# Kernel tuning notes

Measured on AMD Instinct MI355X. Metric: run time of the kernel, lower is better.

## Reference

```python
import jax, jax.numpy as jnp
import numpy as np

B, S, D, H, FFN = 2, 2048, 1024, 8, 4096
DK = D // H            # head key/query dim = 128
VD = 2 * D             # double_v_dim -> v_dim = 2048
DV = VD // H           # per-head value dim = 256
SCALE_BASE = 512.0
EPS = 1e-5


def _dup_interleave(m):
    # (S, d/2) -> (S, d), each column repeated twice adjacently
    return jnp.repeat(m, 2, axis=-1)


def _rotate_every_two(x):
    x1 = x[..., 0::2]
    x2 = x[..., 1::2]
    return jnp.stack((-x2, x1), axis=-1).reshape(x.shape)


def _xpos(x, downscale):
    # x: (B,H,S,d) -- XPOS rotary with length-dependent scale
    d = x.shape[-1]
    pos = jnp.arange(x.shape[-2], dtype=jnp.float32)
    sv = (jnp.arange(0, d, 2, dtype=jnp.float32) + 0.4 * d) / (1.4 * d)  # (d/2,)
    scale = sv[None, :] ** (pos / SCALE_BASE)[:, None]                    # (S, d/2)
    half = d // 2
    inv_freq = 1.0 / (10000.0 ** (jnp.arange(half, dtype=jnp.float32) / half))
    sinusoid = pos[:, None] * inv_freq[None, :]                           # (S, d/2)
    if downscale:
        scale = 1.0 / scale
    sin = _dup_interleave(jnp.sin(sinusoid) * scale)                      # (S, d)
    cos = _dup_interleave(jnp.cos(sinusoid) * scale)
    return x * cos + _rotate_every_two(x) * sin


def _gammas(heads):
    return 1.0 - jnp.exp(jnp.linspace(np.log(1 / 32), np.log(1 / 512), heads)).astype(jnp.float32)


def _layernorm(x, w, b):
    mu = jnp.mean(x, axis=-1, keepdims=True)
    var = jnp.var(x, axis=-1, keepdims=True)
    return (x - mu) * jax.lax.rsqrt(var + EPS) * w + b


def setup_inputs() -> dict:
    key = jax.random.key(0)
    ks = jax.random.split(key, 16)
    sD = 1.0 / np.sqrt(D)
    sF = 1.0 / np.sqrt(FFN)
    return {
        "X": jax.random.normal(ks[0], (B, S, D), jnp.float32),
        "Wq": jax.random.normal(ks[1], (H, D, DK), jnp.float32) * sD,
        "Wk": jax.random.normal(ks[2], (H, D, DK), jnp.float32) * sD,
        "Wv": jax.random.normal(ks[3], (H, D, DV), jnp.float32) * sD,
        "W_G": jax.random.normal(ks[4], (D, VD), jnp.float32) * sD,
        "W_O": jax.random.normal(ks[5], (VD, D), jnp.float32) / np.sqrt(VD),
        "gn_w": jnp.ones((VD,), jnp.float32),
        "gn_b": jnp.zeros((VD,), jnp.float32),
        "ln1_w": jnp.ones((D,), jnp.float32),
        "ln1_b": jnp.zeros((D,), jnp.float32),
        "ln2_w": jnp.ones((D,), jnp.float32),
        "ln2_b": jnp.zeros((D,), jnp.float32),
        "ffn_w1": jax.random.normal(ks[6], (D, FFN), jnp.float32) * sD,
        "ffn_b1": jnp.zeros((FFN,), jnp.float32),
        "ffn_w2": jax.random.normal(ks[7], (FFN, D), jnp.float32) * sF,
        "ffn_b2": jnp.zeros((D,), jnp.float32),
    }


def _retention(Xn, Wq, Wk, Wv, W_G, W_O, gn_w, gn_b):
    # Xn: (B,S,D) pre-normalized input
    Q = jnp.einsum("bsd,hdk->bhsk", Xn, Wq)
    K = jnp.einsum("bsd,hdk->bhsk", Xn, Wk)
    V = jnp.einsum("bsd,hdv->bhsv", Xn, Wv)
    Q = _xpos(Q, downscale=False)
    K = _xpos(K, downscale=True)
    # decay matrix D[h,n,m] = gamma_h^(n-m) for n>=m else 0
    n = jnp.arange(S)[:, None]
    m = jnp.arange(S)[None, :]
    mask = (n >= m)
    exponent = jnp.where(mask, (n - m).astype(jnp.float32), 0.0)
    g = _gammas(H)
    Dmat = jnp.where(mask[None], g[:, None, None] ** exponent[None], 0.0)  # (H,S,S)
    ret = jnp.einsum("bhsk,bhtk->bhst", Q, K) * Dmat[None]
    Y = jnp.einsum("bhst,bhtv->bhsv", ret, V)                              # (B,H,S,DV)
    Y = jnp.transpose(Y, (0, 2, 1, 3))                                     # (B,S,H,DV)
    # GroupNorm(heads, v_dim) applied per token: normalize within each head chunk
    mu = jnp.mean(Y, axis=-1, keepdims=True)
    var = jnp.var(Y, axis=-1, keepdims=True)
    Y = (Y - mu) * jax.lax.rsqrt(var + EPS)
    Y = Y.reshape(B, S, VD) * gn_w + gn_b
    G = Xn @ W_G
    gated = (G * jax.nn.sigmoid(G)) * Y                                     # swish gate
    return gated @ W_O


def reference(X, Wq, Wk, Wv, W_G, W_O, gn_w, gn_b, ln1_w, ln1_b, ln2_w, ln2_b,
              ffn_w1, ffn_b1, ffn_w2, ffn_b2):
    X = _retention(_layernorm(X, ln1_w, ln1_b), Wq, Wk, Wv, W_G, W_O, gn_w, gn_b) + X
    h = _layernorm(X, ln2_w, ln2_b)
    h = jax.nn.gelu(h @ ffn_w1 + ffn_b1, approximate=False) @ ffn_w2 + ffn_b2
    return h + X
```

## Files before the change

kernel.cpp:

```cpp
#include <hip/hip_runtime.h>
#include <hip/hip_bf16.h>

typedef unsigned short u16;
typedef unsigned int   u32;
typedef short short8 __attribute__((ext_vector_type(8)));
typedef float f32x4  __attribute__((ext_vector_type(4)));

__device__ __forceinline__ float b2f(u16 u) { return __uint_as_float(((u32)u) << 16); }
__device__ __forceinline__ u16 f2b(float f) {
    u32 u = __float_as_uint(f);
    u += 0x7FFF + ((u >> 16) & 1);
    return (u16)(u >> 16);
}

typedef const unsigned int __attribute__((address_space(1)))* gas1;
typedef unsigned int __attribute__((address_space(3)))* las3;
__device__ __forceinline__ void async_ld16(const void* g, const void* l) {
    __builtin_amdgcn_global_load_lds((gas1)(unsigned long long)g,
                                     (las3)(unsigned int)(unsigned long long)l,
                                     16, 0, 0);
}

__device__ __forceinline__ void wtrans_body(const float* __restrict__ W, u16* __restrict__ Wt,
                                            int K, int N, int bx, int by, int bz) {
    __shared__ u16 tile[32][36];
    const int k0 = bx * 32, n0 = by * 32;
    const float* Wz = W + (long)bz * K * N;
    u16* Wtz = Wt + (long)bz * K * N;
    const int t = threadIdx.x;
    const int r = t >> 3, c = (t & 7) * 4;
    float4 v = *(const float4*)(Wz + (long)(k0 + r) * N + n0 + c);
    tile[r][c+0] = f2b(v.x); tile[r][c+1] = f2b(v.y);
    tile[r][c+2] = f2b(v.z); tile[r][c+3] = f2b(v.w);
    __syncthreads();
    uint2 pk;
    pk.x = (u32)tile[c+0][r] | ((u32)tile[c+1][r] << 16);
    pk.y = (u32)tile[c+2][r] | ((u32)tile[c+3][r] << 16);
    *(uint2*)(Wtz + (long)(n0 + r) * K + k0 + c) = pk;
}

__device__ __forceinline__ void xtab_body(float4* __restrict__ tab, int blk) {
    int idx = blk * 256 + threadIdx.x;
    int j = idx & 63, s = idx >> 6;
    float sv = (2.f * j + 51.2f) / 179.2f;
    float scale = exp2f(log2f(sv) * ((float)s * (1.f / 512.f)));
    float inv_freq = exp2f((float)j * (-13.287712379549449f / 64.f));
    float ang = (float)s * inv_freq;
    float sn = sinf(ang), cs = cosf(ang);
    tab[idx] = make_float4(cs * scale, sn * scale, cs / scale, sn / scale);
}

__device__ __forceinline__ void ln_body(const float* __restrict__ X,
                                        const float* __restrict__ w,
                                        const float* __restrict__ bb,
                                        u16* __restrict__ out, long row) {
    const int t = threadIdx.x;
    float4 p = ((const float4*)(X + row * 1024))[t];
    float x[4] = { p.x, p.y, p.z, p.w };
    float s = x[0]+x[1]+x[2]+x[3];
    float q = x[0]*x[0]+x[1]*x[1]+x[2]*x[2]+x[3]*x[3];
#pragma unroll
    for (int o = 32; o > 0; o >>= 1) { s += __shfl_down(s, o, 64); q += __shfl_down(q, o, 64); }
    __shared__ float aS[4], aQ[4];
    if ((t & 63) == 0) { aS[t >> 6] = s; aQ[t >> 6] = q; }
    __syncthreads();
    s = aS[0]+aS[1]+aS[2]+aS[3];
    q = aQ[0]+aQ[1]+aQ[2]+aQ[3];
    float mean = s * (1.f/1024.f);
    float var  = q * (1.f/1024.f) - mean*mean;
    float rstd = rsqrtf(var + 1e-5f);
    float4 wv = ((const float4*)w)[t];
    float4 bv = ((const float4*)bb)[t];
    uint2 r;
    r.x = (u32)f2b((x[0]-mean)*rstd*wv.x + bv.x) | ((u32)f2b((x[1]-mean)*rstd*wv.y + bv.y) << 16);
    r.y = (u32)f2b((x[2]-mean)*rstd*wv.z + bv.z) | ((u32)f2b((x[3]-mean)*rstd*wv.w + bv.w) << 16);
    ((uint2*)(out + row * 1024))[t] = r;
}

__global__ __launch_bounds__(256) void prep_k(
    const float* __restrict__ Wq, const float* __restrict__ Wk,
    const float* __restrict__ Wv, const float* __restrict__ WG,
    const float* __restrict__ WO, const float* __restrict__ fw1,
    const float* __restrict__ fw2, const float* __restrict__ X,
    const float* __restrict__ ln1w, const float* __restrict__ ln1b,
    u16* __restrict__ WT, u16* __restrict__ WOT,
    u16* __restrict__ fw1T, u16* __restrict__ fw2T,
    float4* __restrict__ xtab, u16* __restrict__ Xn) {
    const int id = blockIdx.x;
    if (id < 16384) {
        const float* W; u16* Wt; int K, N, bx, by, bz = 0;
        if (id < 1024)       { W=Wq;  Wt=WT;           K=1024; N=128;  int l=id;       bx=l&31;  by=(l>>5)&3; bz=l>>7; }
        else if (id < 2048)  { W=Wk;  Wt=WT+1048576;   K=1024; N=128;  int l=id-1024;  bx=l&31;  by=(l>>5)&3; bz=l>>7; }
        else if (id < 4096)  { W=Wv;  Wt=WT+2097152;   K=1024; N=256;  int l=id-2048;  bx=l&31;  by=(l>>5)&7; bz=l>>8; }
        else if (id < 6144)  { W=WG;  Wt=WT+4194304;   K=1024; N=2048; int l=id-4096;  bx=l&31;  by=l>>5; }
        else if (id < 8192)  { W=WO;  Wt=WOT;          K=2048; N=1024; int l=id-6144;  bx=l&63;  by=l>>6; }
        else if (id < 12288) { W=fw1; Wt=fw1T;         K=1024; N=4096; int l=id-8192;  bx=l&31;  by=l>>5; }
        else                 { W=fw2; Wt=fw2T;         K=4096; N=1024; int l=id-12288; bx=l&127; by=l>>7; }
        wtrans_body(W, Wt, K, N, bx, by, bz);
    } else if (id < 16896) {
        xtab_body(xtab, id - 16384);
    } else {
        ln_body(X, ln1w, ln1b, Xn, id - 16896);
    }
}

__global__ __launch_bounds__(256) void ln2_combine(const float* __restrict__ P,
                                                   const float* __restrict__ X,
                                                   const float* __restrict__ w,
                                                   const float* __restrict__ bb,
                                                   float* __restrict__ X2,
                                                   u16* __restrict__ hb) {
    const long row = blockIdx.x;
    const int t = threadIdx.x;
    const float* p = P + row * 3072;
    float4 a = ((const float4*)p)[t];
    float4 c = ((const float4*)(p + 1024))[t];
    float4 xr = ((const float4*)(X + row * 1024))[t];
    float x[4] = { a.x+c.x+xr.x, a.y+c.y+xr.y, a.z+c.z+xr.z, a.w+c.w+xr.w };
    ((float4*)(X2 + row * 1024))[t] = make_float4(x[0], x[1], x[2], x[3]);
    float s = x[0]+x[1]+x[2]+x[3];
    float q = x[0]*x[0]+x[1]*x[1]+x[2]*x[2]+x[3]*x[3];
#pragma unroll
    for (int o = 32; o > 0; o >>= 1) { s += __shfl_down(s, o, 64); q += __shfl_down(q, o, 64); }
    __shared__ float aS[4], aQ[4];
    if ((t & 63) == 0) { aS[t >> 6] = s; aQ[t >> 6] = q; }
    __syncthreads();
    s = aS[0]+aS[1]+aS[2]+aS[3];
    q = aQ[0]+aQ[1]+aQ[2]+aQ[3];
    float mean = s * (1.f/1024.f);
    float var  = q * (1.f/1024.f) - mean*mean;
    float rstd = rsqrtf(var + 1e-5f);
    float4 wv = ((const float4*)w)[t];
    float4 bv = ((const float4*)bb)[t];
    uint2 r;
    r.x = (u32)f2b((x[0]-mean)*rstd*wv.x + bv.x) | ((u32)f2b((x[1]-mean)*rstd*wv.y + bv.y) << 16);
    r.y = (u32)f2b((x[2]-mean)*rstd*wv.z + bv.z) | ((u32)f2b((x[3]-mean)*rstd*wv.w + bv.w) << 16);
    ((uint2*)(hb + row * 1024))[t] = r;
}

__global__ __launch_bounds__(256) void ffn2_combine(const float* __restrict__ P,
                                                    const float* __restrict__ b2,
                                                    const float* __restrict__ X2,
                                                    float* __restrict__ out) {
    const long row = blockIdx.x;
    const int t = threadIdx.x;
    float4 p0 = ((const float4*)(P + row * 1024))[t];
    float4 p1 = ((const float4*)(P + 16777216 + row * 1024))[t];
    float4 x2 = ((const float4*)(X2 + row * 1024))[t];
    float4 bv = ((const float4*)b2)[t];
    ((float4*)(out + row * 1024))[t] = make_float4(
        p0.x + p1.x + x2.x + bv.x, p0.y + p1.y + x2.y + bv.y,
        p0.z + p1.z + x2.z + bv.z, p0.w + p1.w + x2.w + bv.w);
}

__global__ __launch_bounds__(256) void vtrans(const u16* __restrict__ Vseg, u16* __restrict__ Vt) {
    __shared__ u16 tile[32][36];
    const int s0 = blockIdx.x * 32, v0 = blockIdx.y * 32, z = blockIdx.z;
    const int b = z >> 3, h = z & 7;
    const u16* Vz = Vseg + (long)b * 2048 * 6144 + h * 256;
    u16* Vtz = Vt + (long)z * 256 * 2048;
    const int t = threadIdx.x;
    const int r = t >> 3, c = (t & 7) * 4;
    uint2 ld = *(const uint2*)(Vz + (long)(s0 + r) * 6144 + v0 + c);
    tile[r][c+0] = (u16)(ld.x & 0xFFFF); tile[r][c+1] = (u16)(ld.x >> 16);
    tile[r][c+2] = (u16)(ld.y & 0xFFFF); tile[r][c+3] = (u16)(ld.y >> 16);
    __syncthreads();
    uint2 pk;
    pk.x = (u32)tile[c+0][r] | ((u32)tile[c+1][r] << 16);
    pk.y = (u32)tile[c+2][r] | ((u32)tile[c+3][r] << 16);
    *(uint2*)(Vtz + (long)(v0 + r) * 2048 + s0 + c) = pk;
}

enum { EPI_GELU_BIAS = 2, EPI_QKVG = 4 };

template<int EPI, int PANELS>
__global__ __launch_bounds__(256) void mgemm(
    const u16* __restrict__ A, const u16* __restrict__ Bt, u16* __restrict__ Cv,
    int K, int aStride, long cStride,
    const float* __restrict__ bias) {
    __shared__ __align__(16) u16 As[PANELS * 4096];
    __shared__ __align__(16) u16 Bs[PANELS * 4096];
    const int pid = blockIdx.x;
    const int mb = pid & 31;
    const int nb = pid >> 5;
    const int t = threadIdx.x;
    const int row0 = mb * 128, col0 = nb * 128;
    const int wave = t >> 6, lane = t & 63;
    const int wm = wave >> 1, wn = wave & 1;
    const int quad = lane >> 4, l16 = lane & 15;
    const u16* Ag = A + (long)(row0 + (t >> 2)) * aStride + ((t & 3) * 8);
    const u16* Bg = Bt + (long)(col0 + (t >> 2)) * K + ((t & 3) * 8);
    const long aj = (long)64 * aStride;
    const long bj = (long)64 * K;
    const u32 lo = __builtin_amdgcn_readfirstlane((u32)(wave * 1024));

    f32x4 acc[4][4];
#pragma unroll
    for (int i = 0; i < 4; i++)
#pragma unroll
        for (int j = 0; j < 4; j++) acc[i][j] = (f32x4){0.f, 0.f, 0.f, 0.f};

    for (int k0 = 0; k0 < K; k0 += PANELS * 32) {
#pragma unroll
        for (int h = 0; h < PANELS; h++) {
            const u16* Agh = Ag + k0 + h * 32;
            const u16* Bgh = Bg + k0 + h * 32;
            async_ld16(Agh,      (const char*)As + h*8192 + lo);
            async_ld16(Agh + aj, (const char*)As + h*8192 + 4096 + lo);
            async_ld16(Bgh,      (const char*)Bs + h*8192 + lo);
            async_ld16(Bgh + bj, (const char*)Bs + h*8192 + 4096 + lo);
        }
        __syncthreads();
#pragma unroll
        for (int h = 0; h < PANELS; h++) {
            short8 af[4], bf[4];
#pragma unroll
            for (int mt = 0; mt < 4; mt++)
                af[mt] = *(const short8*)(As + h*4096 + (wm*64 + mt*16 + l16) * 32 + quad*8);
#pragma unroll
            for (int nt = 0; nt < 4; nt++)
                bf[nt] = *(const short8*)(Bs + h*4096 + (wn*64 + nt*16 + l16) * 32 + quad*8);
#pragma unroll
            for (int mt = 0; mt < 4; mt++)
#pragma unroll
                for (int nt = 0; nt < 4; nt++)
                    acc[mt][nt] = __builtin_amdgcn_mfma_f32_16x16x32_bf16(af[mt], bf[nt], acc[mt][nt], 0, 0, 0);
        }
        __syncthreads();
    }

#pragma unroll
    for (int mt = 0; mt < 4; mt++) {
#pragma unroll
        for (int reg = 0; reg < 4; reg++) {
            int r = row0 + wm*64 + mt*16 + quad*4 + reg;
#pragma unroll
            for (int nt = 0; nt < 4; nt++) {
                int c = col0 + wn*64 + nt*16 + l16;
                float v = acc[mt][nt][reg];
                if constexpr (EPI == EPI_GELU_BIAS) {
                    v += bias[c];
                    v = 0.5f * v * (1.f + erff(v * 0.70710678118654752f));
                } else if constexpr (EPI == EPI_QKVG) {
                    if (c < 2048) {
                        int j = (c & 127) >> 1;
                        float4 tb = ((const float4*)bias)[((r & 2047) << 6) + j];
                        float cs = (c < 1024) ? tb.x : tb.z;
                        float sn = (c < 1024) ? tb.y : tb.w;
                        float partner = __shfl_xor(v, 1, 64);
                        v = v * cs + ((c & 1) ? partner : -partner) * sn;
                    }
                }
                Cv[(long)r * cStride + c] = f2b(v);
            }
        }
    }
}

__global__ __launch_bounds__(256) void mgemm_sk(
    const u16* __restrict__ A, const u16* __restrict__ Bt, float* __restrict__ P,
    int K, int kHalf, int aStride, long pRowStride, long sliceOff) {
    __shared__ __align__(16) u16 As[2 * 4096];
    __shared__ __align__(16) u16 Bs[2 * 4096];
    const int pid = blockIdx.x;
    const int mb = pid & 31;
    const int nb = (pid & 255) >> 5;
    const int slice = pid >> 8;
    const int t = threadIdx.x;
    const int row0 = mb * 128, col0 = nb * 128;
    const int wave = t >> 6, lane = t & 63;
    const int wm = wave >> 1, wn = wave & 1;
    const int quad = lane >> 4, l16 = lane & 15;
    const u16* Ag = A + (long)(row0 + (t >> 2)) * aStride + ((t & 3) * 8);
    const u16* Bg = Bt + (long)(col0 + (t >> 2)) * K + ((t & 3) * 8);
    const long aj = (long)64 * aStride;
    const long bj = (long)64 * K;
    const u32 lo = __builtin_amdgcn_readfirstlane((u32)(wave * 1024));

    f32x4 acc[4][4];
#pragma unroll
    for (int i = 0; i < 4; i++)
#pragma unroll
        for (int j = 0; j < 4; j++) acc[i][j] = (f32x4){0.f, 0.f, 0.f, 0.f};

    const int kBeg = slice * kHalf, kEnd = kBeg + kHalf;
    for (int k0 = kBeg; k0 < kEnd; k0 += 64) {
#pragma unroll
        for (int h = 0; h < 2; h++) {
            const u16* Agh = Ag + k0 + h * 32;
            const u16* Bgh = Bg + k0 + h * 32;
            async_ld16(Agh,      (const char*)As + h*8192 + lo);
            async_ld16(Agh + aj, (const char*)As + h*8192 + 4096 + lo);
            async_ld16(Bgh,      (const char*)Bs + h*8192 + lo);
            async_ld16(Bgh + bj, (const char*)Bs + h*8192 + 4096 + lo);
        }
        __syncthreads();
#pragma unroll
        for (int h = 0; h < 2; h++) {
            short8 af[4], bf[4];
#pragma unroll
            for (int mt = 0; mt < 4; mt++)
                af[mt] = *(const short8*)(As + h*4096 + (wm*64 + mt*16 + l16) * 32 + quad*8);
#pragma unroll
            for (int nt = 0; nt < 4; nt++)
                bf[nt] = *(const short8*)(Bs + h*4096 + (wn*64 + nt*16 + l16) * 32 + quad*8);
#pragma unroll
            for (int mt = 0; mt < 4; mt++)
#pragma unroll
                for (int nt = 0; nt < 4; nt++)
                    acc[mt][nt] = __builtin_amdgcn_mfma_f32_16x16x32_bf16(af[mt], bf[nt], acc[mt][nt], 0, 0, 0);
        }
        __syncthreads();
    }

    float* Pb = P + slice * sliceOff;
#pragma unroll
    for (int mt = 0; mt < 4; mt++) {
#pragma unroll
        for (int reg = 0; reg < 4; reg++) {
            int r = row0 + wm*64 + mt*16 + quad*4 + reg;
#pragma unroll
            for (int nt = 0; nt < 4; nt++) {
                int c = col0 + wn*64 + nt*16 + l16;
                Pb[(long)r * pRowStride + c] = acc[mt][nt][reg];
            }
        }
    }
}

__global__ __launch_bounds__(256) void retention_mfma(
    u16* __restrict__ QKVG, const u16* __restrict__ Vt,
    const float* __restrict__ gnw, const float* __restrict__ gnb) {
    __shared__ __align__(16) u16 Qs[4][64][32];
    __shared__ __align__(16) u16 Ks[2][4][32][32];
    __shared__ __align__(16) u16 Vs[2][256][32];
    __shared__ u16 Ss[64][40];
    const int id = blockIdx.x;
    const int halfg = id >> 8, r5 = id & 255;
    const int bh = r5 >> 4, i16 = r5 & 15;
    const int tile = halfg ? i16 : 31 - i16;
    const int b = bh >> 3, h = bh & 7;
    const int t = threadIdx.x;
    const int wave = t >> 6, lane = t & 63, quad = lane >> 4, l16 = lane & 15;
    const u32 lo = __builtin_amdgcn_readfirstlane((u32)(wave * 1024));
    const u16* Qbase = QKVG + (long)b * 2048 * 6144 + h * 128;
    const u16* Kbase = Qbase + 1024;
    const u16* Vbase = Vt + (long)(b * 8 + h) * 256 * 2048;
    u16* Gseg = QKVG + (long)b * 2048 * 6144 + 4096 + h * 256;

    float g = 1.f - expf(-3.4657359027997265f + (-0.3960841031771116f) * (float)h);
    float log2g = log2f(g);
    const float gi16 = exp2f(log2g * -16.f);
    const float gi32 = gi16 * gi16;
    const float gf[4] = {1.f, g, g*g, g*g*g};
    const int srow0 = tile*64 + wave*16 + quad*4;
    float drun = exp2f(log2g * (float)(srow0 - l16));

    auto issueKV = [&](int jt, int buf) {
#pragma unroll
        for (int i = 0; i < 2; i++) {
            int c = t + i * 256;
            int ks = c >> 7, row = (c >> 2) & 31, cb = c & 3;
            async_ld16(Kbase + (long)(jt*32 + row) * 6144 + ks*32 + cb*8,
                       (const char*)Ks + buf*8192 + i*4096 + lo);
        }
#pragma unroll
        for (int i = 0; i < 4; i++) {
            int c = t + i * 256;
            int row = c >> 2, cb = c & 3;
            async_ld16(Vbase + (long)row * 2048 + jt*32 + cb*8,
                       (const char*)Vs + buf*16384 + i*4096 + lo);
        }
    };

#pragma unroll
    for (int i = 0; i < 4; i++) {
        int c = t + i * 256;
        int ks = c >> 8, row = (c >> 2) & 63, cb = c & 3;
        async_ld16(Qbase + (long)(tile*64 + row) * 6144 + ks*32 + cb*8,
                   (const char*)Qs + i*4096 + lo);
    }
    issueKV(0, 0);

    float gw[16], gbv[16];
#pragma unroll
    for (int nt = 0; nt < 16; nt++) {
        gw[nt]  = gnw[h*256 + nt*16 + l16];
        gbv[nt] = gnb[h*256 + nt*16 + l16];
    }
    f32x4 oacc[16];
#pragma unroll
    for (int nt = 0; nt < 16; nt++) oacc[nt] = (f32x4){0.f, 0.f, 0.f, 0.f};
    __syncthreads();

    const int njt = 2 * tile + 2;
    for (int jt = 0; jt < njt; jt++) {
        const int cur = jt & 1;
        if (jt + 1 < njt) issueKV(jt + 1, cur ^ 1);
        f32x4 s0 = (f32x4){0.f,0.f,0.f,0.f}, s1 = (f32x4){0.f,0.f,0.f,0.f};
#pragma unroll
        for (int ks = 0; ks < 4; ks++) {
            short8 aq = *(const short8*)&Qs[ks][wave*16 + l16][quad*8];
            short8 b0 = *(const short8*)&Ks[cur][ks][l16][quad*8];
            short8 b1 = *(const short8*)&Ks[cur][ks][16 + l16][quad*8];
            s0 = __builtin_amdgcn_mfma_f32_16x16x32_bf16(aq, b0, s0, 0, 0, 0);
            s1 = __builtin_amdgcn_mfma_f32_16x16x32_bf16(aq, b1, s1, 0, 0, 0);
        }
#pragma unroll
        for (int reg = 0; reg < 4; reg++) {
            int srow = srow0 + reg;
            int tc0 = jt*32 + l16, tc1 = tc0 + 16;
            float dbase = drun * gf[reg];
            float d0 = (srow >= tc0) ? dbase : 0.f;
            float d1 = (srow >= tc1) ? dbase * gi16 : 0.f;
            Ss[wave*16 + quad*4 + reg][l16]      = f2b(s0[reg] * d0);
            Ss[wave*16 + quad*4 + reg][16 + l16] = f2b(s1[reg] * d1);
        }
        drun *= gi32;
        short8 as = *(const short8*)&Ss[wave*16 + l16][quad*8];
#pragma unroll
        for (int nt = 0; nt < 16; nt++) {
            short8 bv = *(const short8*)&Vs[cur][nt*16 + l16][quad*8];
            oacc[nt] = __builtin_amdgcn_mfma_f32_16x16x32_bf16(as, bv, oacc[nt], 0, 0, 0);
        }
        __syncthreads();
    }

#pragma unroll
    for (int reg = 0; reg < 4; reg++) {
        float s = 0.f, q = 0.f;
#pragma unroll
        for (int nt = 0; nt < 16; nt++) { float v = oacc[nt][reg]; s += v; q += v*v; }
#pragma unroll
        for (int m = 1; m < 16; m <<= 1) { s += __shfl_xor(s, m, 16); q += __shfl_xor(q, m, 16); }
        float mean = s * (1.f/256.f);
        float var  = q * (1.f/256.f) - mean*mean;
        float rstd = rsqrtf(var + 1e-5f);
        int srow = srow0 + reg;
        u16* grow = Gseg + (long)srow * 6144;
#pragma unroll
        for (int nt = 0; nt < 16; nt++) {
            float gval = b2f(grow[nt*16 + l16]);
            float y = (oacc[nt][reg] - mean) * rstd * gw[nt] + gbv[nt];
            float sg = gval / (1.f + expf(-gval));
            grow[nt*16 + l16] = f2b(sg * y);
        }
    }
}

extern "C" void kernel_launch(void* const* d_in, const int* in_sizes, int n_in,
                              void* d_out, int out_size, void* d_ws, size_t ws_size,
                              hipStream_t stream) {
    (void)in_sizes; (void)n_in; (void)out_size; (void)ws_size;
    const float* X    = (const float*)d_in[0];
    const float* Wq   = (const float*)d_in[1];
    const float* Wk   = (const float*)d_in[2];
    const float* Wv   = (const float*)d_in[3];
    const float* WG   = (const float*)d_in[4];
    const float* WO   = (const float*)d_in[5];
    const float* gnw  = (const float*)d_in[6];
    const float* gnb  = (const float*)d_in[7];
    const float* ln1w = (const float*)d_in[8];
    const float* ln1b = (const float*)d_in[9];
    const float* ln2w = (const float*)d_in[10];
    const float* ln2b = (const float*)d_in[11];
    const float* fw1  = (const float*)d_in[12];
    const float* fb1  = (const float*)d_in[13];
    const float* fw2  = (const float*)d_in[14];
    const float* fb2  = (const float*)d_in[15];

    constexpr int D = 1024, FFN = 4096;
    constexpr int M = 4096;
    constexpr long MB = 1048576;

    char* ws = (char*)d_ws;
    u16* WT   = (u16*)(ws + 0*MB);
    u16* WOT  = (u16*)(ws + 12*MB);
    u16* fw1T = (u16*)(ws + 16*MB);
    u16* fw2T = (u16*)(ws + 24*MB);
    u16*   QKVG = (u16*)(ws + 32*MB);
    u16*   Xn   = (u16*)(ws + 80*MB);
    float4* xtab= (float4*)(ws + 88*MB);
    u16*   Vt   = (u16*)(ws + 80*MB);
    float* X2   = (float*)(ws + 80*MB);
    u16*   hb   = (u16*)(ws + 0*MB);
    u16*   mid  = (u16*)(ws + 32*MB);
    float* PF   = (float*)(ws + 0*MB);

    prep_k<<<20992, 256, 0, stream>>>(Wq, Wk, Wv, WG, WO, fw1, fw2, X, ln1w, ln1b,
                                      WT, WOT, fw1T, fw2T, xtab, Xn);
    mgemm<EPI_QKVG, 1><<<1536, 256, 0, stream>>>(
        Xn, WT, QKVG, D, D, 6144, (const float*)xtab);
    vtrans<<<dim3(64, 8, 16), 256, 0, stream>>>(QKVG + 2048, Vt);
    retention_mfma<<<512, 256, 0, stream>>>(QKVG, Vt, gnw, gnb);
    mgemm_sk<<<512, 256, 0, stream>>>(
        QKVG + 4096, WOT, (float*)QKVG, 2048, 1024, 6144, 3072, 1024);
    ln2_combine<<<M, 256, 0, stream>>>((const float*)QKVG, X, ln2w, ln2b, X2, hb);
    mgemm<EPI_GELU_BIAS, 2><<<1024, 256, 0, stream>>>(
        hb, fw1T, mid, D, D, FFN, fb1);
    mgemm_sk<<<512, 256, 0, stream>>>(
        mid, fw2T, PF, 4096, 2048, 4096, 1024, 16777216);
    ffn2_combine<<<M, 256, 0, stream>>>(PF, fb2, X2, (float*)d_out);
}
```

Before: 472.3 us.

## Fuse V transpose into QKVG GEMM epilogue and use faster GELU/sigmoid

The QKVG GEMM epilogue now writes V tiles directly in transposed layout to a separate Vt buffer, which removes the standalone vtrans kernel and its round trip through memory. The exact erf GELU is replaced with a sigmoid-based polynomial approximation, and the swish sigmoid uses exp2f. The approximation adds some numerical error in GELU and assumes the relocated Vt buffer does not overlap live data.

```diff
diff --git a/kernel.cpp b/kernel.cpp
--- a/kernel.cpp
+++ b/kernel.cpp
@@ -11,6 +11,12 @@
     u32 u = __float_as_uint(f);
     u += 0x7FFF + ((u >> 16) & 1);
     return (u16)(u >> 16);
+}
+__device__ __forceinline__ float gelu_fast(float v) {
+    float a = v * (2.302118f + 0.102953f * v * v);
+    a = fminf(a, 120.f);
+    float e = exp2f(a);
+    return v * e / (1.f + e);
 }
 
 typedef const unsigned int __attribute__((address_space(1)))* gas1;
@@ -153,31 +159,13 @@
         p0.z + p1.z + x2.z + bv.z, p0.w + p1.w + x2.w + bv.w);
 }
 
-__global__ __launch_bounds__(256) void vtrans(const u16* __restrict__ Vseg, u16* __restrict__ Vt) {
-    __shared__ u16 tile[32][36];
-    const int s0 = blockIdx.x * 32, v0 = blockIdx.y * 32, z = blockIdx.z;
-    const int b = z >> 3, h = z & 7;
-    const u16* Vz = Vseg + (long)b * 2048 * 6144 + h * 256;
-    u16* Vtz = Vt + (long)z * 256 * 2048;
-    const int t = threadIdx.x;
-    const int r = t >> 3, c = (t & 7) * 4;
-    uint2 ld = *(const uint2*)(Vz + (long)(s0 + r) * 6144 + v0 + c);
-    tile[r][c+0] = (u16)(ld.x & 0xFFFF); tile[r][c+1] = (u16)(ld.x >> 16);
-    tile[r][c+2] = (u16)(ld.y & 0xFFFF); tile[r][c+3] = (u16)(ld.y >> 16);
-    __syncthreads();
-    uint2 pk;
-    pk.x = (u32)tile[c+0][r] | ((u32)tile[c+1][r] << 16);
-    pk.y = (u32)tile[c+2][r] | ((u32)tile[c+3][r] << 16);
-    *(uint2*)(Vtz + (long)(v0 + r) * 2048 + s0 + c) = pk;
-}
-
 enum { EPI_GELU_BIAS = 2, EPI_QKVG = 4 };
 
 template<int EPI, int PANELS>
 __global__ __launch_bounds__(256) void mgemm(
     const u16* __restrict__ A, const u16* __restrict__ Bt, u16* __restrict__ Cv,
     int K, int aStride, long cStride,
-    const float* __restrict__ bias) {
+    const float* __restrict__ bias, u16* __restrict__ Vt) {
     __shared__ __align__(16) u16 As[PANELS * 4096];
     __shared__ __align__(16) u16 Bs[PANELS * 4096];
     const int pid = blockIdx.x;
@@ -229,6 +217,27 @@
         __syncthreads();
     }
 
+    if constexpr (EPI == EPI_QKVG) {
+        if (col0 >= 2048 && col0 < 4096) {
+            const int bq = row0 >> 11;
+            const int sb = (row0 & 2047) + wm*64 + quad*4;
+#pragma unroll
+            for (int mt = 0; mt < 4; mt++) {
+#pragma unroll
+                for (int nt = 0; nt < 4; nt++) {
+                    int vc = (col0 - 2048) + wn*64 + nt*16 + l16;
+                    u16* dst = Vt + ((long)((bq << 3) + (vc >> 8)) * 256 + (vc & 255)) * 2048
+                                  + sb + mt*16;
+                    uint2 pk;
+                    pk.x = (u32)f2b(acc[mt][nt][0]) | ((u32)f2b(acc[mt][nt][1]) << 16);
+                    pk.y = (u32)f2b(acc[mt][nt][2]) | ((u32)f2b(acc[mt][nt][3]) << 16);
+                    *(uint2*)dst = pk;
+                }
+            }
+            return;
+        }
+    }
+
 #pragma unroll
     for (int mt = 0; mt < 4; mt++) {
 #pragma unroll
@@ -239,8 +248,7 @@
                 int c = col0 + wn*64 + nt*16 + l16;
                 float v = acc[mt][nt][reg];
                 if constexpr (EPI == EPI_GELU_BIAS) {
-                    v += bias[c];
-                    v = 0.5f * v * (1.f + erff(v * 0.70710678118654752f));
+                    v = gelu_fast(v + bias[c]);
                 } else if constexpr (EPI == EPI_QKVG) {
                     if (c < 2048) {
                         int j = (c & 127) >> 1;
@@ -442,7 +450,7 @@
         for (int nt = 0; nt < 16; nt++) {
             float gval = b2f(grow[nt*16 + l16]);
             float y = (oacc[nt][reg] - mean) * rstd * gw[nt] + gbv[nt];
-            float sg = gval / (1.f + expf(-gval));
+            float sg = gval / (1.f + exp2f(-1.4426950408889634f * gval));
             grow[nt*16 + l16] = f2b(sg * y);
         }
     }
@@ -481,7 +489,7 @@
     u16*   QKVG = (u16*)(ws + 32*MB);
     u16*   Xn   = (u16*)(ws + 80*MB);
     float4* xtab= (float4*)(ws + 88*MB);
-    u16*   Vt   = (u16*)(ws + 80*MB);
+    u16*   Vt   = (u16*)(ws + 90*MB);
     float* X2   = (float*)(ws + 80*MB);
     u16*   hb   = (u16*)(ws + 0*MB);
     u16*   mid  = (u16*)(ws + 32*MB);
@@ -490,14 +498,13 @@
     prep_k<<<20992, 256, 0, stream>>>(Wq, Wk, Wv, WG, WO, fw1, fw2, X, ln1w, ln1b,
                                       WT, WOT, fw1T, fw2T, xtab, Xn);
     mgemm<EPI_QKVG, 1><<<1536, 256, 0, stream>>>(
-        Xn, WT, QKVG, D, D, 6144, (const float*)xtab);
-    vtrans<<<dim3(64, 8, 16), 256, 0, stream>>>(QKVG + 2048, Vt);
+        Xn, WT, QKVG, D, D, 6144, (const float*)xtab, Vt);
     retention_mfma<<<512, 256, 0, stream>>>(QKVG, Vt, gnw, gnb);
     mgemm_sk<<<512, 256, 0, stream>>>(
         QKVG + 4096, WOT, (float*)QKVG, 2048, 1024, 6144, 3072, 1024);
     ln2_combine<<<M, 256, 0, stream>>>((const float*)QKVG, X, ln2w, ln2b, X2, hb);
     mgemm<EPI_GELU_BIAS, 2><<<1024, 256, 0, stream>>>(
-        hb, fw1T, mid, D, D, FFN, fb1);
+        hb, fw1T, mid, D, D, FFN, fb1, nullptr);
     mgemm_sk<<<512, 256, 0, stream>>>(
         mid, fw2T, PF, 4096, 2048, 4096, 1024, 16777216);
     ffn2_combine<<<M, 256, 0, stream>>>(PF, fb2, X2, (float*)d_out);
```

Result: faster. 446.1 us (-5.5%).
